# Kernel tuning notes

Hardware: AMD Instinct MI355X
Metric: run time of the kernel (lower is better)

Reference implementation:

```python
import jax, jax.numpy as jnp
import numpy as np

B, H, W = 128, 32, 32
INF = 1e9
EPS = 1e-6  # strictly positive weights -> dist strictly decreases along backtrack (no tie cycles)
OFFS = np.array([(-1, -1), (-1, 0), (-1, 1), (0, -1), (0, 1), (1, -1), (1, 0), (1, 1)], dtype=np.int32)


def _neighbor_min(d):
    # d: [B,H,W] -> per-cell min over 8-neighborhood (INF outside the grid)
    p = jnp.pad(d, ((0, 0), (1, 1), (1, 1)), constant_values=INF)
    sh = jnp.stack([p[:, 1 + dr:1 + dr + H, 1 + dc:1 + dc + W] for dr, dc in OFFS], axis=0)
    return jnp.min(sh, axis=0)


def solve(weights, source, target):
    """Dijkstra/A*(h=0)-equivalent shortest path on an 8-connected grid.
    Entering cell v costs weights[v]; returns a [B,H,W] 0/1 mask of the optimal path
    (source and target cells included). Computed exactly via Bellman-Ford relaxation
    (H*W sweeps >= max hop count) followed by greedy min-dist backtracking.
    """
    w = weights + EPS
    b = jnp.arange(B)
    sr, sc = source[:, 0], source[:, 1]
    ws = w[b, sr, sc]
    dist0 = jnp.full((B, H, W), INF, w.dtype).at[b, sr, sc].set(ws)

    def bf_step(dist, _):
        return jnp.minimum(dist, w + _neighbor_min(dist)), None

    dist, _ = jax.lax.scan(bf_step, dist0, None, length=H * W)

    dist_flat = dist.reshape(B, H * W)
    offs = jnp.asarray(OFFS)  # [8,2]
    hw = jnp.array([H, W], offs.dtype)

    def bt_step(carry, _):
        pos, mask, done = carry            # pos [B,2], mask [B,H,W], done [B]
        r, c = pos[:, 0], pos[:, 1]
        mask = mask.at[b, r, c].max((~done).astype(mask.dtype))
        done = done | ((r == sr) & (c == sc))
        cand = pos[:, None, :] + offs[None]               # [B,8,2]
        valid = ((cand >= 0) & (cand < hw)).all(-1)       # [B,8]
        cr = jnp.clip(cand[..., 0], 0, H - 1)
        cc = jnp.clip(cand[..., 1], 0, W - 1)
        dvals = jnp.take_along_axis(dist_flat, cr * W + cc, axis=1)
        dvals = jnp.where(valid, dvals, INF)
        j = jnp.argmin(dvals, axis=1)                     # predecessor = min-dist neighbor
        nxt = jnp.stack([cr[b, j], cc[b, j]], axis=1)
        pos = jnp.where(done[:, None], pos, nxt)
        return (pos, mask, done), None

    mask0 = jnp.zeros((B, H, W), weights.dtype)
    done0 = jnp.zeros((B,), bool)
    (_, paths, _), _ = jax.lax.scan(bt_step, (target.astype(offs.dtype), mask0, done0), None, length=H * W)
    return paths


def setup_inputs() -> dict:
    key = jax.random.key(0)
    k1, k2, k3 = jax.random.split(key, 3)
    return {
        "weights": jax.random.uniform(k1, (B, H, W), jnp.float32),
        "source": jax.random.randint(k2, (B, 2), 0, H),
        "target": jax.random.randint(k3, (B, 2), 0, H),
    }


def reference(weights, source, target):
    # BBAStar.forward: paths come straight from a_star_batch (the autograd.Function
    # forward is identity on paths); exp_nodes is solver-internal bookkeeping and is
    # not part of the math being differentiated, so we return the path masks.
    return solve(weights, source, target)
```

## Files before the change

### kernel.cpp

```cpp
#include <hip/hip_runtime.h>

#define GH 32
#define GW 32
#define PITCH 34
#define NPAD (PITCH * PITCH)
#define INFV 1000000000.0f
#define EPSV 1e-6f

__global__ __launch_bounds__(256)
void bbastar_kernel(const float* __restrict__ weights,
                    const int* __restrict__ source,
                    const int* __restrict__ target,
                    float* __restrict__ out) {
    __shared__ float d[NPAD];
    __shared__ int flags[2][4];

    const int b   = blockIdx.x;
    const int tid = threadIdx.x;
    const int r   = tid >> 3;
    const int q   = tid & 7;
    const int c0  = q << 2;
    const int base = (r + 1) * PITCH + (c0 + 1);

    const int sr = source[2 * b];
    const int sc = source[2 * b + 1];

    const float4 w4 = ((const float4*)(weights + b * (GH * GW)))[tid];
    float w[4] = { w4.x + EPSV, w4.y + EPSV, w4.z + EPSV, w4.w + EPSV };

    ((float4*)(out + b * (GH * GW)))[tid] = make_float4(0.f, 0.f, 0.f, 0.f);

    for (int i = tid; i < NPAD; i += 256) d[i] = INFV;
    __syncthreads();
    float myd[4];
    #pragma unroll
    for (int k = 0; k < 4; ++k) {
        const bool is_src = (r == sr) && (c0 + k == sc);
        myd[k] = is_src ? w[k] : INFV;
        if (is_src) d[base + k] = w[k];
    }
    __syncthreads();

    for (int it = 0; it < 2048; ++it) {
        float t[6], btm[6];
        #pragma unroll
        for (int k = 0; k < 6; ++k) {
            t[k]   = d[base - PITCH - 1 + k];
            btm[k] = d[base + PITCH - 1 + k];
        }
        const float lft = d[base - 1];
        const float rgt = d[base + 4];

        bool ch = false;
        if ((it & 1) == 0) {
            #pragma unroll
            for (int k = 0; k < 4; ++k) {
                const float lnb = (k == 0) ? lft : myd[k - 1];
                const float rnb = (k == 3) ? rgt : myd[k + 1];
                const float nmin = fminf(fminf(fminf(t[k], t[k + 1]), fminf(t[k + 2], btm[k])),
                                         fminf(fminf(btm[k + 1], btm[k + 2]), fminf(lnb, rnb)));
                const float nd = w[k] + nmin;
                if (nd < myd[k]) { myd[k] = nd; d[base + k] = nd; ch = true; }
            }
        } else {
            #pragma unroll
            for (int k = 3; k >= 0; --k) {
                const float lnb = (k == 0) ? lft : myd[k - 1];
                const float rnb = (k == 3) ? rgt : myd[k + 1];
                const float nmin = fminf(fminf(fminf(t[k], t[k + 1]), fminf(t[k + 2], btm[k])),
                                         fminf(fminf(btm[k + 1], btm[k + 2]), fminf(lnb, rnb)));
                const float nd = w[k] + nmin;
                if (nd < myd[k]) { myd[k] = nd; d[base + k] = nd; ch = true; }
            }
        }

        const unsigned long long bal = __ballot(ch);
        if ((tid & 63) == 0) flags[it & 1][tid >> 6] = (bal != 0ULL) ? 1 : 0;
        __syncthreads();
        const int any = flags[it & 1][0] | flags[it & 1][1] |
                        flags[it & 1][2] | flags[it & 1][3];
        if (!any) break;
    }

    if (tid == 0) {
        const int drr[8] = {-1, -1, -1,  0, 0,  1, 1, 1};
        const int dcc[8] = {-1,  0,  1, -1, 1, -1, 0, 1};
        int pr = target[2 * b];
        int pc = target[2 * b + 1];
        float* ob = out + b * (GH * GW);
        for (int step = 0; step < GH * GW; ++step) {
            ob[pr * GW + pc] = 1.0f;
            if (pr == sr && pc == sc) break;
            float best = INFV;
            int bj = 0;
            #pragma unroll
            for (int j = 0; j < 8; ++j) {
                const float v = d[(pr + drr[j] + 1) * PITCH + (pc + dcc[j] + 1)];
                if (v < best) { best = v; bj = j; }
            }
            pr += drr[bj];
            pc += dcc[bj];
        }
    }
}

extern "C" void kernel_launch(void* const* d_in, const int* in_sizes, int n_in,
                              void* d_out, int out_size, void* d_ws, size_t ws_size,
                              hipStream_t stream) {
    const float* weights = (const float*)d_in[0];
    const int*   source  = (const int*)d_in[1];
    const int*   target  = (const int*)d_in[2];
    float*       out     = (float*)d_out;
    const int B = in_sizes[0] / (GH * GW);
    bbastar_kernel<<<B, 256, 0, stream>>>(weights, source, target, out);
}
```

Measured before the change: 80.47 us.

## Use single-wavefront blocks with 4x4 register tiles and bidirectional sweeps

Each block now runs as one 64-thread wavefront. Every thread owns a 4x4 tile held in registers and does a forward then a backward Gauss-Seidel sweep over it in each iteration, writing the tile to shared memory once per iteration. Running a single wave removes the cross-wave flag array, and the ballot alone now serves as the convergence test. More propagation happens per barrier, so fewer iterations should be needed, at the cost of more register pressure and less parallelism per block.

```diff
diff --git a/kernel.cpp b/kernel.cpp
--- a/kernel.cpp
+++ b/kernel.cpp
@@ -7,78 +7,100 @@
 #define INFV 1000000000.0f
 #define EPSV 1e-6f
 
-__global__ __launch_bounds__(256)
+
+#define RELAX(i,j) {                                                          \
+    const float ul = ((i)==0) ? top[(j)]   : (((j)==0) ? lft[(i)-1] : t[(i)-1][(j)-1]); \
+    const float uu = ((i)==0) ? top[(j)+1] : t[(i)-1][(j)];                    \
+    const float ur = ((i)==0) ? top[(j)+2] : (((j)==3) ? rgt[(i)-1] : t[(i)-1][(j)+1]); \
+    const float ll = ((j)==0) ? lft[(i)]   : t[(i)][(j)-1];                    \
+    const float rr = ((j)==3) ? rgt[(i)]   : t[(i)][(j)+1];                    \
+    const float dl = ((i)==3) ? bot[(j)]   : (((j)==0) ? lft[(i)+1] : t[(i)+1][(j)-1]); \
+    const float dd = ((i)==3) ? bot[(j)+1] : t[(i)+1][(j)];                    \
+    const float dr = ((i)==3) ? bot[(j)+2] : (((j)==3) ? rgt[(i)+1] : t[(i)+1][(j)+1]); \
+    const float nmin = fminf(fminf(fminf(ul, uu), fminf(ur, ll)),             \
+                             fminf(fminf(rr, dl), fminf(dd, dr)));            \
+    const float nd = w[i][j] + nmin;                                          \
+    if (nd < t[i][j]) { t[i][j] = nd; ch = true; }                            \
+}
+
+__global__ __launch_bounds__(64)
 void bbastar_kernel(const float* __restrict__ weights,
                     const int* __restrict__ source,
                     const int* __restrict__ target,
                     float* __restrict__ out) {
     __shared__ float d[NPAD];
-    __shared__ int flags[2][4];
 
     const int b   = blockIdx.x;
     const int tid = threadIdx.x;
-    const int r   = tid >> 3;
-    const int q   = tid & 7;
-    const int c0  = q << 2;
-    const int base = (r + 1) * PITCH + (c0 + 1);
+    const int tr  = tid >> 3;
+    const int tc  = tid & 7;
+    const int r0  = tr << 2;
+    const int c0  = tc << 2;
+    const int base = (r0 + 1) * PITCH + (c0 + 1);
 
     const int sr = source[2 * b];
     const int sc = source[2 * b + 1];
 
-    const float4 w4 = ((const float4*)(weights + b * (GH * GW)))[tid];
-    float w[4] = { w4.x + EPSV, w4.y + EPSV, w4.z + EPSV, w4.w + EPSV };
+    float w[4][4], t[4][4];
+    const float* wb = weights + b * (GH * GW);
+    #pragma unroll
+    for (int i = 0; i < 4; ++i) {
+        const float4 v = *(const float4*)(wb + (r0 + i) * GW + c0);
+        w[i][0] = v.x + EPSV; w[i][1] = v.y + EPSV;
+        w[i][2] = v.z + EPSV; w[i][3] = v.w + EPSV;
+    }
 
-    ((float4*)(out + b * (GH * GW)))[tid] = make_float4(0.f, 0.f, 0.f, 0.f);
+    float4* ob4 = (float4*)(out + b * (GH * GW));
+    #pragma unroll
+    for (int k = 0; k < 4; ++k) ob4[tid + 64 * k] = make_float4(0.f, 0.f, 0.f, 0.f);
 
-    for (int i = tid; i < NPAD; i += 256) d[i] = INFV;
-    __syncthreads();
-    float myd[4];
+    for (int i = tid; i < NPAD; i += 64) d[i] = INFV;
     #pragma unroll
-    for (int k = 0; k < 4; ++k) {
-        const bool is_src = (r == sr) && (c0 + k == sc);
-        myd[k] = is_src ? w[k] : INFV;
-        if (is_src) d[base + k] = w[k];
-    }
+    for (int i = 0; i < 4; ++i)
+        #pragma unroll
+        for (int j = 0; j < 4; ++j) t[i][j] = INFV;
     __syncthreads();
 
-    for (int it = 0; it < 2048; ++it) {
-        float t[6], btm[6];
+    #pragma unroll
+    for (int i = 0; i < 4; ++i)
+        #pragma unroll
+        for (int j = 0; j < 4; ++j)
+            if (sr == r0 + i && sc == c0 + j) {
+                t[i][j] = w[i][j];
+                d[base + i * PITCH + j] = w[i][j];
+            }
+    __syncthreads();
+
+    for (int it = 0; it < 1024; ++it) {
+        float top[6], bot[6], lft[4], rgt[4];
         #pragma unroll
         for (int k = 0; k < 6; ++k) {
-            t[k]   = d[base - PITCH - 1 + k];
-            btm[k] = d[base + PITCH - 1 + k];
+            top[k] = d[base - PITCH - 1 + k];
+            bot[k] = d[base + 4 * PITCH - 1 + k];
         }
-        const float lft = d[base - 1];
-        const float rgt = d[base + 4];
+        #pragma unroll
+        for (int i = 0; i < 4; ++i) {
+            lft[i] = d[base + i * PITCH - 1];
+            rgt[i] = d[base + i * PITCH + 4];
+        }
 
         bool ch = false;
-        if ((it & 1) == 0) {
+        #pragma unroll
+        for (int i = 0; i < 4; ++i)
             #pragma unroll
-            for (int k = 0; k < 4; ++k) {
-                const float lnb = (k == 0) ? lft : myd[k - 1];
-                const float rnb = (k == 3) ? rgt : myd[k + 1];
-                const float nmin = fminf(fminf(fminf(t[k], t[k + 1]), fminf(t[k + 2], btm[k])),
-                                         fminf(fminf(btm[k + 1], btm[k + 2]), fminf(lnb, rnb)));
-                const float nd = w[k] + nmin;
-                if (nd < myd[k]) { myd[k] = nd; d[base + k] = nd; ch = true; }
-            }
-        } else {
+            for (int j = 0; j < 4; ++j) RELAX(i, j)
+        #pragma unroll
+        for (int i = 3; i >= 0; --i)
             #pragma unroll
-            for (int k = 3; k >= 0; --k) {
-                const float lnb = (k == 0) ? lft : myd[k - 1];
-                const float rnb = (k == 3) ? rgt : myd[k + 1];
-                const float nmin = fminf(fminf(fminf(t[k], t[k + 1]), fminf(t[k + 2], btm[k])),
-                                         fminf(fminf(btm[k + 1], btm[k + 2]), fminf(lnb, rnb)));
-                const float nd = w[k] + nmin;
-                if (nd < myd[k]) { myd[k] = nd; d[base + k] = nd; ch = true; }
-            }
-        }
+            for (int j = 3; j >= 0; --j) RELAX(i, j)
 
-        const unsigned long long bal = __ballot(ch);
-        if ((tid & 63) == 0) flags[it & 1][tid >> 6] = (bal != 0ULL) ? 1 : 0;
+        #pragma unroll
+        for (int i = 0; i < 4; ++i)
+            #pragma unroll
+            for (int j = 0; j < 4; ++j) d[base + i * PITCH + j] = t[i][j];
+
+        const bool any = (__ballot(ch) != 0ULL);
         __syncthreads();
-        const int any = flags[it & 1][0] | flags[it & 1][1] |
-                        flags[it & 1][2] | flags[it & 1][3];
         if (!any) break;
     }
 
@@ -112,5 +134,5 @@
     const int*   target  = (const int*)d_in[2];
     float*       out     = (float*)d_out;
     const int B = in_sizes[0] / (GH * GW);
-    bbastar_kernel<<<B, 256, 0, stream>>>(weights, source, target, out);
+    bbastar_kernel<<<B, 64, 0, stream>>>(weights, source, target, out);
 }
```

Measured after the change: 81.09 us. No clear change (+0.8%).

## Replace Jacobi-style relaxation with wavefront directional sweeps in one wavefront

Applied to the files above, without the earlier changes.

Reworks the relaxation so that one 64-lane wavefront runs directional sweeps. Lanes hold whole rows or columns in registers and alternate between row and column passes in forward and reverse directions. Neighbouring values are exchanged with shuffles, so each pass carries distance updates across the full grid and needs far fewer outer iterations. The block shrinks to 64 threads, and the cross-wave flag reduction is replaced by a single ballot. In exchange, half the lanes do padding work, the 32-element register arrays raise register pressure, and each pass is a long serial dependency chain.

```diff
diff --git a/kernel.cpp b/kernel.cpp
--- a/kernel.cpp
+++ b/kernel.cpp
@@ -2,84 +2,102 @@
 
 #define GH 32
 #define GW 32
-#define PITCH 34
-#define NPAD (PITCH * PITCH)
+#define P  33
 #define INFV 1000000000.0f
 #define EPSV 1e-6f
 
-__global__ __launch_bounds__(256)
+
+#define STEP(J, VB) {                                                      \
+    const float vj = v[J];                                                 \
+    const float u1 = __shfl(VB, tid - 1), d1 = __shfl(VB, tid + 1);        \
+    const float nmin = fminf(fminf(fminf(cu, cd), fminf(u0c, d0c)),        \
+                             fminf(fminf(u1, d1), fminf(ca, VB)));         \
+    const float nd = wv[J] + nmin;                                         \
+    float vn = vj;                                                         \
+    if (nd < vn) { vn = nd; ch = true; }                                   \
+    const float mu = __shfl(vn, tid - 1), md = __shfl(vn, tid + 1);        \
+    const float nd2 = wv[J] + fminf(mu, md);      \
+    if (nd2 < vn) { vn = nd2; ch = true; }                                 \
+    v[J] = vn;                                                             \
+    cu = mu; cd = md; ca = vn; u0c = u1; d0c = d1;                         \
+}
+
+__global__ __launch_bounds__(64)
 void bbastar_kernel(const float* __restrict__ weights,
                     const int* __restrict__ source,
                     const int* __restrict__ target,
                     float* __restrict__ out) {
-    __shared__ float d[NPAD];
-    __shared__ int flags[2][4];
+    __shared__ float d[GH * P];
+    __shared__ float wl[GH * P];
 
     const int b   = blockIdx.x;
     const int tid = threadIdx.x;
-    const int r   = tid >> 3;
-    const int q   = tid & 7;
-    const int c0  = q << 2;
-    const int base = (r + 1) * PITCH + (c0 + 1);
-
     const int sr = source[2 * b];
     const int sc = source[2 * b + 1];
 
-    const float4 w4 = ((const float4*)(weights + b * (GH * GW)))[tid];
-    float w[4] = { w4.x + EPSV, w4.y + EPSV, w4.z + EPSV, w4.w + EPSV };
+    float4* ob4 = (float4*)(out + b * (GH * GW));
+    #pragma unroll
+    for (int k = 0; k < 4; ++k) ob4[tid + 64 * k] = make_float4(0.f, 0.f, 0.f, 0.f);
 
-    ((float4*)(out + b * (GH * GW)))[tid] = make_float4(0.f, 0.f, 0.f, 0.f);
-
-    for (int i = tid; i < NPAD; i += 256) d[i] = INFV;
-    __syncthreads();
-    float myd[4];
+    const float* wb = weights + b * (GH * GW);
     #pragma unroll
     for (int k = 0; k < 4; ++k) {
-        const bool is_src = (r == sr) && (c0 + k == sc);
-        myd[k] = is_src ? w[k] : INFV;
-        if (is_src) d[base + k] = w[k];
+        const int idx = tid + 64 * k;
+        const float4 v4 = ((const float4*)wb)[idx];
+        const int e = idx * 4;
+        const int r = e >> 5, c = e & 31;
+        wl[r * P + c    ] = v4.x + EPSV;
+        wl[r * P + c + 1] = v4.y + EPSV;
+        wl[r * P + c + 2] = v4.z + EPSV;
+        wl[r * P + c + 3] = v4.w + EPSV;
     }
+    for (int i = tid; i < GH * P; i += 64) d[i] = INFV;
+    __syncthreads();
+    if (tid == 0) d[sr * P + sc] = wl[sr * P + sc];
     __syncthreads();
 
-    for (int it = 0; it < 2048; ++it) {
-        float t[6], btm[6];
-        #pragma unroll
-        for (int k = 0; k < 6; ++k) {
-            t[k]   = d[base - PITCH - 1 + k];
-            btm[k] = d[base + PITCH - 1 + k];
-        }
-        const float lft = d[base - 1];
-        const float rgt = d[base + 4];
-
-        bool ch = false;
-        if ((it & 1) == 0) {
+    for (int pass = 0; pass < 256; ++pass) {
+        const int  mode = pass & 3;
+        const bool colm = mode & 1;
+        float v[32], wv[32];
+        if (tid < 32) {
             #pragma unroll
-            for (int k = 0; k < 4; ++k) {
-                const float lnb = (k == 0) ? lft : myd[k - 1];
-                const float rnb = (k == 3) ? rgt : myd[k + 1];
-                const float nmin = fminf(fminf(fminf(t[k], t[k + 1]), fminf(t[k + 2], btm[k])),
-                                         fminf(fminf(btm[k + 1], btm[k + 2]), fminf(lnb, rnb)));
-                const float nd = w[k] + nmin;
-                if (nd < myd[k]) { myd[k] = nd; d[base + k] = nd; ch = true; }
+            for (int j = 0; j < 32; ++j) {
+                const int a = colm ? (j * P + tid) : (tid * P + j);
+                v[j]  = d[a];
+                wv[j] = wl[a];
             }
         } else {
             #pragma unroll
-            for (int k = 3; k >= 0; --k) {
-                const float lnb = (k == 0) ? lft : myd[k - 1];
-                const float rnb = (k == 3) ? rgt : myd[k + 1];
-                const float nmin = fminf(fminf(fminf(t[k], t[k + 1]), fminf(t[k + 2], btm[k])),
-                                         fminf(fminf(btm[k + 1], btm[k + 2]), fminf(lnb, rnb)));
-                const float nd = w[k] + nmin;
-                if (nd < myd[k]) { myd[k] = nd; d[base + k] = nd; ch = true; }
+            for (int j = 0; j < 32; ++j) { v[j] = INFV; wv[j] = INFV; }
+        }
+
+        bool ch = false;
+        float cu = INFV, cd = INFV, ca = INFV, u0c, d0c;
+        if (!(mode & 2)) {
+            u0c = __shfl(v[0], tid - 1); d0c = __shfl(v[0], tid + 1);
+            #pragma unroll
+            for (int s = 0; s < 32; ++s) {
+                const float vb = (s < 31) ? v[s + 1] : INFV;
+                STEP(s, vb)
+            }
+        } else {
+            u0c = __shfl(v[31], tid - 1); d0c = __shfl(v[31], tid + 1);
+            #pragma unroll
+            for (int s = 0; s < 32; ++s) {
+                const int j = 31 - s;
+                const float vb = (j > 0) ? v[j - 1] : INFV;
+                STEP(j, vb)
             }
         }
 
-        const unsigned long long bal = __ballot(ch);
-        if ((tid & 63) == 0) flags[it & 1][tid >> 6] = (bal != 0ULL) ? 1 : 0;
+        if (tid < 32) {
+            #pragma unroll
+            for (int j = 0; j < 32; ++j)
+                d[colm ? (j * P + tid) : (tid * P + j)] = v[j];
+        }
         __syncthreads();
-        const int any = flags[it & 1][0] | flags[it & 1][1] |
-                        flags[it & 1][2] | flags[it & 1][3];
-        if (!any) break;
+        if (__ballot(ch) == 0ULL) break;
     }
 
     if (tid == 0) {
@@ -95,8 +113,12 @@
             int bj = 0;
             #pragma unroll
             for (int j = 0; j < 8; ++j) {
-                const float v = d[(pr + drr[j] + 1) * PITCH + (pc + dcc[j] + 1)];
-                if (v < best) { best = v; bj = j; }
+                const int nr = pr + drr[j], nc = pc + dcc[j];
+                const bool ok = (nr >= 0) & (nr < GH) & (nc >= 0) & (nc < GW);
+                const int cr = min(max(nr, 0), GH - 1);
+                const int cc = min(max(nc, 0), GW - 1);
+                const float vv = ok ? d[cr * P + cc] : INFV;
+                if (vv < best) { best = vv; bj = j; }
             }
             pr += drr[bj];
             pc += dcc[bj];
@@ -112,5 +134,5 @@
     const int*   target  = (const int*)d_in[2];
     float*       out     = (float*)d_out;
     const int B = in_sizes[0] / (GH * GW);
-    bbastar_kernel<<<B, 256, 0, stream>>>(weights, source, target, out);
+    bbastar_kernel<<<B, 64, 0, stream>>>(weights, source, target, out);
 }
```

Result: slower. 140.0 us (+73.9%).
